# Kernel optimization log

Hardware: AMD Instinct MI355X
Metric: run time of the kernel (lower is better)

Reference implementation:

```python
import jax, jax.numpy as jnp
import numpy as np

N = 20000      # nodes
E = 160000     # edges (before self loops)
IN = 128       # in_channels (== edge_dim)
H = 8          # heads
C = 64         # out_channels per head
NEG_SLOPE = 0.2


def setup_inputs() -> dict:
    key = jax.random.key(0)
    ks = jax.random.split(key, 8)
    s_in = np.float32(1.0 / np.sqrt(IN))
    s_att = np.float32(1.0 / np.sqrt(C))
    return {
        "x": jax.random.normal(ks[0], (N, IN), jnp.float32),
        "edge_index": jax.random.randint(ks[1], (2, E), 0, N, dtype=jnp.int32),
        "edge_attr": jax.random.normal(ks[2], (E, IN), jnp.float32),
        "Wl": jax.random.normal(ks[3], (IN, H * C), jnp.float32) * s_in,
        "Wr": jax.random.normal(ks[4], (IN, H * C), jnp.float32) * s_in,
        "We": jax.random.normal(ks[5], (IN, H * C), jnp.float32) * s_in,
        "att": jax.random.normal(ks[6], (H, C), jnp.float32) * s_att,
        "bias": jnp.zeros((H * C,), jnp.float32),
    }


def reference(x, edge_index, edge_attr, Wl, Wr, We, att, bias):
    n = x.shape[0]
    e = edge_attr.shape[0]
    src, dst = edge_index[0], edge_index[1]

    # add self loops; self-loop edge_attr = per-target-node mean of incoming
    # edge attrs (PyG fill_value='mean'); nodes with no in-edges get zeros.
    cnt = jax.ops.segment_sum(jnp.ones((e,), x.dtype), dst, num_segments=n)
    loop_attr = jax.ops.segment_sum(edge_attr, dst, num_segments=n) / jnp.maximum(cnt, 1.0)[:, None]
    loops = jnp.arange(n, dtype=src.dtype)
    src_f = jnp.concatenate([src, loops])          # [E+N]
    dst_f = jnp.concatenate([dst, loops])          # [E+N]
    ea = jnp.concatenate([edge_attr, loop_attr], axis=0)  # [E+N, IN]

    xl = (x @ Wl).reshape(n, H, C)   # source projection
    xr = (x @ Wr).reshape(n, H, C)   # target projection
    xe = (ea @ We).reshape(-1, H, C)  # edge projection

    # GATv2 score: att . LeakyReLU(xl_j + xr_i + xe)
    m = jax.nn.leaky_relu(xl[src_f] + xr[dst_f] + xe, NEG_SLOPE)  # [E+N, H, C]
    logits = jnp.einsum('ehc,hc->eh', m, att)                      # [E+N, H]

    # segment softmax over incoming edges of each target node
    lmax = jax.ops.segment_max(logits, dst_f, num_segments=n)      # [N, H]
    p = jnp.exp(logits - lmax[dst_f])
    denom = jax.ops.segment_sum(p, dst_f, num_segments=n)
    alpha = p / denom[dst_f]                                       # [E+N, H]

    # weighted scatter-add aggregation of source features
    out = jax.ops.segment_sum(alpha[:, :, None] * xl[src_f], dst_f, num_segments=n)
    return out.reshape(n, H * C) + bias
```

## Files before the change

### kernel.cpp

```cpp
#include <hip/hip_runtime.h>

#define N_NODES 20000
#define E_EDGES 160000
#define IN_CH 128
#define H_HEADS 8
#define C_CH 64
#define HC 512
#define M_TOT (E_EDGES + N_NODES)
#define NEG_SLOPE 0.2f
#define NCHUNK ((N_NODES + 255) / 256)

typedef __attribute__((ext_vector_type(8))) short bf16x8;
typedef __attribute__((ext_vector_type(4))) float f32x4;

__device__ __forceinline__ unsigned short f2bf(float f) {
    unsigned u = __float_as_uint(f);
    unsigned r = (u + 0x7FFFu + ((u >> 16) & 1u)) >> 16;
    return (unsigned short)r;
}
__device__ __forceinline__ float bf2f(unsigned short s) {
    return __uint_as_float((unsigned)s << 16);
}
__device__ __forceinline__ float bfx(const bf16x8& v0, const bf16x8& v1, int idx) {
    return bf2f((unsigned short)((idx < 8) ? v0[idx] : v1[idx - 8]));
}

#define GLOAD_LDS16(gsrc, ldst) \
    __builtin_amdgcn_global_load_lds((const __attribute__((address_space(1))) void*)(gsrc), \
                                     (__attribute__((address_space(3))) void*)(ldst), 16, 0, 0)

__global__ void k_deg(const int* __restrict__ ei, int* __restrict__ deg) {
    int e = blockIdx.x * blockDim.x + threadIdx.x;
    if (e >= E_EDGES) return;
    atomicAdd(&deg[ei[E_EDGES + e]], 1);
}

__global__ void k_scan1(const int* __restrict__ deg, int* __restrict__ bsum) {
    __shared__ int red[256];
    int tid = threadIdx.x;
    int i = blockIdx.x * 256 + tid;
    red[tid] = (i < N_NODES) ? deg[i] + 1 : 0;
    __syncthreads();
    for (int off = 128; off > 0; off >>= 1) {
        if (tid < off) red[tid] += red[tid + off];
        __syncthreads();
    }
    if (tid == 0) bsum[blockIdx.x] = red[0];
}

__global__ void k_scan2(const int* __restrict__ bsum, int* __restrict__ boff) {
    if (threadIdx.x == 0) {
        int run = 0;
        for (int b = 0; b < NCHUNK; ++b) { boff[b] = run; run += bsum[b]; }
    }
}

__global__ void k_scan3(const int* __restrict__ deg, const int* __restrict__ boff,
                        int* __restrict__ rowptr, int* __restrict__ cursor,
                        int* __restrict__ eidx, int* __restrict__ src_s,
                        int* __restrict__ dst_s) {
    __shared__ int buf[256];
    int tid = threadIdx.x;
    int i = blockIdx.x * 256 + tid;
    int v = (i < N_NODES) ? deg[i] + 1 : 0;
    buf[tid] = v;
    __syncthreads();
    for (int off = 1; off < 256; off <<= 1) {
        int tv = (tid >= off) ? buf[tid - off] : 0;
        __syncthreads();
        buf[tid] += tv;
        __syncthreads();
    }
    if (i < N_NODES) {
        int excl = boff[blockIdx.x] + buf[tid] - v;
        rowptr[i] = excl;
        eidx[excl] = E_EDGES + i;
        src_s[excl] = i;
        dst_s[excl] = i;
        cursor[i] = excl + 1;
        if (i == N_NODES - 1) rowptr[N_NODES] = excl + v;
    }
}

__global__ void k_fill(const int* __restrict__ ei, int* __restrict__ cursor,
                       int* __restrict__ eidx, int* __restrict__ src_s,
                       int* __restrict__ dst_s) {
    int e = blockIdx.x * blockDim.x + threadIdx.x;
    if (e >= E_EDGES) return;
    int d = ei[E_EDGES + e];
    int slot = atomicAdd(&cursor[d], 1);
    eidx[slot] = e;
    src_s[slot] = ei[e];
    dst_s[slot] = d;
}

__global__ void k_prep(const int* __restrict__ rowptr, const int* __restrict__ eidx,
                       const float* __restrict__ ea, unsigned short* __restrict__ eab) {
    int node = (blockIdx.x * blockDim.x + threadIdx.x) >> 6;
    int lane = threadIdx.x & 63;
    if (node >= N_NODES) return;
    int beg = rowptr[node], end = rowptr[node + 1];
    int cnt = end - beg - 1;
    float s0 = 0.f, s1 = 0.f;
    if (beg + 1 < end) {
        const float* p_nxt = ea + (size_t)eidx[beg + 1] * 128 + lane;
        for (int p = beg + 1; p < end; ++p) {
            const float* cur = p_nxt;
            if (p + 1 < end) p_nxt = ea + (size_t)eidx[p + 1] * 128 + lane;
            float v0 = cur[0], v1 = cur[64];
            s0 += v0; s1 += v1;
            eab[(size_t)p * 128 + lane] = f2bf(v0);
            eab[(size_t)p * 128 + 64 + lane] = f2bf(v1);
        }
    }
    float inv = 1.f / fmaxf((float)cnt, 1.f);
    eab[(size_t)beg * 128 + lane] = f2bf(s0 * inv);
    eab[(size_t)beg * 128 + 64 + lane] = f2bf(s1 * inv);
}

__global__ void k_trans3(const float* __restrict__ Wl, const float* __restrict__ Wr,
                         const float* __restrict__ We,
                         unsigned short* __restrict__ WlT, unsigned short* __restrict__ WrT,
                         unsigned short* __restrict__ WeT) {
    int idx = blockIdx.x * blockDim.x + threadIdx.x;
    if (idx >= HC * IN_CH) return;
    int m = blockIdx.y;
    const float* W = (m == 0) ? Wl : (m == 1) ? Wr : We;
    unsigned short* WT = (m == 0) ? WlT : (m == 1) ? WrT : WeT;
    int n = idx >> 7, k = idx & 127;
    WT[idx] = f2bf(W[(size_t)k * HC + n]);
}

__global__ void k_gemm2(const float* __restrict__ A,
                        const unsigned short* __restrict__ WlT,
                        const unsigned short* __restrict__ WrT,
                        unsigned short* __restrict__ xlb, unsigned short* __restrict__ xrb,
                        int M) {
    __shared__ short As[64 * 128];
    int row0 = blockIdx.x * 64;
    int sel = blockIdx.y >> 1;
    const unsigned short* BT = sel ? WrT : WlT;
    unsigned short* Cb = sel ? xrb : xlb;
    int t = threadIdx.x;
    {
        int row = t >> 2, c0 = (t & 3) * 32;
        int gr = row0 + row;
        int sw = (row & 7) << 4;
        const float* src = A + (size_t)gr * 128 + c0;
        #pragma unroll
        for (int i = 0; i < 4; ++i) {
            bf16x8 v;
            if (gr < M) {
                const float4* p = (const float4*)(src + i * 8);
                float4 f0 = p[0], f1 = p[1];
                v[0] = f2bf(f0.x); v[1] = f2bf(f0.y); v[2] = f2bf(f0.z); v[3] = f2bf(f0.w);
                v[4] = f2bf(f1.x); v[5] = f2bf(f1.y); v[6] = f2bf(f1.z); v[7] = f2bf(f1.w);
            } else {
                #pragma unroll
                for (int j = 0; j < 8; ++j) v[j] = 0;
            }
            int off = row * 256 + (((c0 + i * 8) * 2) ^ sw);
            *(bf16x8*)((char*)As + off) = v;
        }
    }
    __syncthreads();

    int w = t >> 6, l = t & 63;
    int lr = l & 15, lk = l >> 4;
    int col0 = (blockIdx.y & 1) * 256 + w * 64;

    f32x4 acc[4][4];
    #pragma unroll
    for (int mi = 0; mi < 4; ++mi)
        #pragma unroll
        for (int fj = 0; fj < 4; ++fj)
            #pragma unroll
            for (int q = 0; q < 4; ++q) acc[mi][fj][q] = 0.f;

    #pragma unroll
    for (int k0 = 0; k0 < 4; ++k0) {
        bf16x8 a4[4];
        #pragma unroll
        for (int mi = 0; mi < 4; ++mi) {
            int row = mi * 16 + lr;
            int off = row * 256 + ((k0 * 64 + lk * 16) ^ ((row & 7) << 4));
            a4[mi] = *(const bf16x8*)((const char*)As + off);
        }
        #pragma unroll
        for (int fj = 0; fj < 4; ++fj) {
            bf16x8 b = *(const bf16x8*)(BT + (size_t)(col0 + fj * 16 + lr) * 128 + k0 * 32 + lk * 8);
            #pragma unroll
            for (int mi = 0; mi < 4; ++mi)
                acc[mi][fj] = __builtin_amdgcn_mfma_f32_16x16x32_bf16(a4[mi], b, acc[mi][fj], 0, 0, 0);
        }
    }
    #pragma unroll
    for (int mi = 0; mi < 4; ++mi) {
        #pragma unroll
        for (int reg = 0; reg < 4; ++reg) {
            int r = row0 + mi * 16 + lk * 4 + reg;
            if (r < M) {
                unsigned short* cp = Cb + (size_t)r * 512 + col0 + lr;
                #pragma unroll
                for (int fj = 0; fj < 4; ++fj) cp[fj * 16] = f2bf(acc[mi][fj][reg]);
            }
        }
    }
}

#define PREF(R, CB, SLOT) { \
    int s_ = s_src[R], d_ = s_dst[R]; \
    const bf16x8* xp_ = (const bf16x8*)(xlb + (size_t)s_ * 512 + (CB) + q * 16); \
    pa0[SLOT] = xp_[0]; pa1[SLOT] = xp_[1]; \
    const bf16x8* rp_ = (const bf16x8*)(xrb + (size_t)d_ * 512 + (CB) + q * 16); \
    pb0[SLOT] = rp_[0]; pb1[SLOT] = rp_[1]; }

__global__ void k_fused(const int* __restrict__ src_s, const int* __restrict__ dst_s,
                        const int* __restrict__ rowptr,
                        const unsigned short* __restrict__ eab,
                        const unsigned short* __restrict__ WeT,
                        const unsigned short* __restrict__ xlb,
                        const unsigned short* __restrict__ xrb,
                        const float* __restrict__ att, const float* __restrict__ bias,
                        float* __restrict__ logits, float* __restrict__ out) {
    __shared__ short As[64 * 128];
    __shared__ float xeT[4][16][68];
    __shared__ float att_s[512];
    __shared__ float lg[64][8];
    __shared__ int s_src[64], s_dst[64];
    __shared__ int own_node[64], own_beg[64], own_len[64];
    __shared__ int n_own;
    int row0 = blockIdx.x * 64;
    int t = threadIdx.x;

    if (t == 0) n_own = 0;
    __syncthreads();

    {
        int l = t & 63;
        int c_base = (t >> 6) * 4;
        #pragma unroll
        for (int i = 0; i < 4; ++i) {
            int c = c_base + i;
            int row_local = c * 4 + (l >> 4);
            int grow = row0 + row_local;
            if (grow > M_TOT - 1) grow = M_TOT - 1;
            int chunk = (l & 15) ^ (row_local & 7);
            const char* src = (const char*)eab + (size_t)grow * 256 + chunk * 16;
            char* dst = (char*)As + c * 1024;
            GLOAD_LDS16(src, dst);
        }
    }

    if (t < 64) {
        int p = row0 + t;
        int s = 0, d = 0;
        if (p < M_TOT) {
            s = src_s[p]; d = dst_s[p];
            int pb = rowptr[d], pe = rowptr[d + 1];
            if (pb == p && pe <= row0 + 64) {
                int idx = atomicAdd(&n_own, 1);
                own_node[idx] = d; own_beg[idx] = t; own_len[idx] = pe - pb;
            }
        }
        s_src[t] = s; s_dst[t] = d;
    }
    att_s[t] = att[t];
    att_s[t + 256] = att[t + 256];

    asm volatile("s_waitcnt vmcnt(0)");
    __syncthreads();

    int w = t >> 6, l = t & 63;
    int lr = l & 15, lk = l >> 4;
    int eloc = l >> 2, q = l & 3;
    int cb0 = w * 128;

    bf16x8 pa0[2], pa1[2], pb0[2], pb1[2];
    f32x4 acc[4][4];

    PREF(eloc, cb0, 0);

    #pragma unroll
    for (int hh = 0; hh < 2; ++hh) {
        int cb = cb0 + hh * 64;
        int h = w * 2 + hh;

        #pragma unroll
        for (int mi = 0; mi < 4; ++mi)
            #pragma unroll
            for (int fj = 0; fj < 4; ++fj)
                #pragma unroll
                for (int qq = 0; qq < 4; ++qq) acc[mi][fj][qq] = 0.f;

        #pragma unroll
        for (int k0 = 0; k0 < 4; ++k0) {
            bf16x8 a4[4];
            #pragma unroll
            for (int mi = 0; mi < 4; ++mi) {
                int row = mi * 16 + lr;
                int off = row * 256 + ((k0 * 64 + lk * 16) ^ ((row & 7) << 4));
                a4[mi] = *(const bf16x8*)((const char*)As + off);
            }
            #pragma unroll
            for (int fj = 0; fj < 4; ++fj) {
                bf16x8 b = *(const bf16x8*)(WeT + (size_t)(cb + fj * 16 + lr) * 128 + k0 * 32 + lk * 8);
                #pragma unroll
                for (int mi = 0; mi < 4; ++mi)
                    acc[mi][fj] = __builtin_amdgcn_mfma_f32_16x16x32_bf16(a4[mi], b, acc[mi][fj], 0, 0, 0);
            }
        }

        #pragma unroll
        for (int mi = 0; mi < 4; ++mi) {
            if (mi < 3) { PREF(mi * 16 + 16 + eloc, cb, (mi + 1) & 1); }
            else if (hh == 0) { PREF(eloc, cb + 64, 0); }

            #pragma unroll
            for (int fj = 0; fj < 4; ++fj)
                #pragma unroll
                for (int reg = 0; reg < 4; ++reg)
                    xeT[w][lk * 4 + reg][fj * 16 + lr] = acc[mi][fj][reg];

            const bf16x8 ca0 = pa0[mi & 1], ca1 = pa1[mi & 1];
            const bf16x8 cb0v = pb0[mi & 1], cb1v = pb1[mi & 1];

            float sum = 0.f;
            #pragma unroll
            for (int sg = 0; sg < 4; ++sg) {
                float4 xe4 = *(const float4*)&xeT[w][eloc][q * 16 + sg * 4];
                float4 av  = *(const float4*)&att_s[cb + q * 16 + sg * 4];
                float v0 = xe4.x + bfx(ca0, ca1, sg * 4 + 0) + bfx(cb0v, cb1v, sg * 4 + 0);
                float v1 = xe4.y + bfx(ca0, ca1, sg * 4 + 1) + bfx(cb0v, cb1v, sg * 4 + 1);
                float v2 = xe4.z + bfx(ca0, ca1, sg * 4 + 2) + bfx(cb0v, cb1v, sg * 4 + 2);
                float v3 = xe4.w + bfx(ca0, ca1, sg * 4 + 3) + bfx(cb0v, cb1v, sg * 4 + 3);
                v0 = (v0 > 0.f) ? v0 : v0 * NEG_SLOPE;
                v1 = (v1 > 0.f) ? v1 : v1 * NEG_SLOPE;
                v2 = (v2 > 0.f) ? v2 : v2 * NEG_SLOPE;
                v3 = (v3 > 0.f) ? v3 : v3 * NEG_SLOPE;
                sum = fmaf(av.x, v0, sum);
                sum = fmaf(av.y, v1, sum);
                sum = fmaf(av.z, v2, sum);
                sum = fmaf(av.w, v3, sum);
            }
            sum += __shfl_xor(sum, 1, 64);
            sum += __shfl_xor(sum, 2, 64);
            if (q == 0) {
                int rloc = mi * 16 + eloc;
                lg[rloc][h] = sum;
                int p = row0 + rloc;
                if (p < M_TOT) logits[(size_t)p * 8 + h] = sum;
            }
        }
    }
    __syncthreads();

    {
        int lane = t & 63;
        int h = lane >> 3;
        for (int o = w; o < n_own; o += 4) {
            int d = own_node[o], rb = own_beg[o], len = own_len[o];
            float m = -3.4e38f;
            for (int j = 0; j < len; ++j) m = fmaxf(m, lg[rb + j][h]);
            float den = 0.f;
            for (int j = 0; j < len; ++j) den += __expf(lg[rb + j][h] - m);
            float rden = 1.f / den;
            float ac[8] = {};
            bf16x8 v_nxt = *(const bf16x8*)(xlb + (size_t)s_src[rb] * 512 + lane * 8);
            for (int j = 0; j < len; ++j) {
                bf16x8 v = v_nxt;
                if (j + 1 < len)
                    v_nxt = *(const bf16x8*)(xlb + (size_t)s_src[rb + j + 1] * 512 + lane * 8);
                float alpha = __expf(lg[rb + j][h] - m) * rden;
                #pragma unroll
                for (int jj = 0; jj < 8; ++jj) ac[jj] = fmaf(alpha, bf2f((unsigned short)v[jj]), ac[jj]);
            }
            float4* op = (float4*)(out + (size_t)d * 512 + lane * 8);
            const float4* bp = (const float4*)(bias + lane * 8);
            float4 bv0 = bp[0], bv1 = bp[1];
            float4 r0 = { ac[0] + bv0.x, ac[1] + bv0.y, ac[2] + bv0.z, ac[3] + bv0.w };
            float4 r1 = { ac[4] + bv1.x, ac[5] + bv1.y, ac[6] + bv1.z, ac[7] + bv1.w };
            op[0] = r0; op[1] = r1;
        }
    }
}

__global__ void k_cleanup(const int* __restrict__ rowptr, const int* __restrict__ src_s,
                          const float* __restrict__ logits,
                          const unsigned short* __restrict__ xlb, const float* __restrict__ bias,
                          float* __restrict__ out) {
    int node = (blockIdx.x * blockDim.x + threadIdx.x) >> 6;
    int lane = threadIdx.x & 63;
    if (node >= N_NODES) return;
    int beg = rowptr[node], end = rowptr[node + 1];
    if ((beg >> 6) == ((end - 1) >> 6)) return;
    int h = lane >> 3;

    float m = -3.4e38f;
    for (int p = beg; p < end; ++p) m = fmaxf(m, logits[(size_t)p * 8 + h]);
    float den = 0.f;
    for (int p = beg; p < end; ++p) den += __expf(logits[(size_t)p * 8 + h] - m);
    float rden = 1.f / den;

    float acc[8] = {};
    bf16x8 v_nxt = *(const bf16x8*)(xlb + (size_t)src_s[beg] * 512 + lane * 8);
    for (int p = beg; p < end; ++p) {
        bf16x8 v = v_nxt;
        float lgv = logits[(size_t)p * 8 + h];
        if (p + 1 < end)
            v_nxt = *(const bf16x8*)(xlb + (size_t)src_s[p + 1] * 512 + lane * 8);
        float alpha = __expf(lgv - m) * rden;
        #pragma unroll
        for (int j = 0; j < 8; ++j) acc[j] = fmaf(alpha, bf2f((unsigned short)v[j]), acc[j]);
    }
    float4* op = (float4*)(out + (size_t)node * 512 + lane * 8);
    const float4* bp = (const float4*)(bias + lane * 8);
    float4 bv0 = bp[0], bv1 = bp[1];
    float4 r0 = { acc[0] + bv0.x, acc[1] + bv0.y, acc[2] + bv0.z, acc[3] + bv0.w };
    float4 r1 = { acc[4] + bv1.x, acc[5] + bv1.y, acc[6] + bv1.z, acc[7] + bv1.w };
    op[0] = r0; op[1] = r1;
}

extern "C" void kernel_launch(void* const* d_in, const int* in_sizes, int n_in,
                              void* d_out, int out_size, void* d_ws, size_t ws_size,
                              hipStream_t stream) {
    const float* x    = (const float*)d_in[0];
    const int*   ei   = (const int*)d_in[1];
    const float* ea   = (const float*)d_in[2];
    const float* Wl   = (const float*)d_in[3];
    const float* Wr   = (const float*)d_in[4];
    const float* We   = (const float*)d_in[5];
    const float* att  = (const float*)d_in[6];
    const float* bias = (const float*)d_in[7];
    float* out = (float*)d_out;

    unsigned short* xlb = (unsigned short*)d_ws;
    unsigned short* xrb = xlb + (size_t)N_NODES * HC;
    unsigned short* WlT = xrb + (size_t)N_NODES * HC;
    unsigned short* WrT = WlT + HC * IN_CH;
    unsigned short* WeT = WrT + HC * IN_CH;
    unsigned short* eab = WeT + HC * IN_CH;
    float* logits    = (float*)(eab + (size_t)M_TOT * IN_CH);
    int* deg         = (int*)(logits + (size_t)M_TOT * 8);
    int* rowptr      = deg + N_NODES;
    int* cursor      = rowptr + N_NODES + 1;
    int* eidx        = cursor + N_NODES;
    int* src_s       = eidx + M_TOT;
    int* dst_s       = src_s + M_TOT;
    int* bsum        = dst_s + M_TOT;
    int* boff        = bsum + NCHUNK;

    const int B = 256;
    hipMemsetAsync(deg, 0, N_NODES * sizeof(int), stream);
    k_deg<<<(E_EDGES + B - 1) / B, B, 0, stream>>>(ei, deg);
    k_scan1<<<NCHUNK, B, 0, stream>>>(deg, bsum);
    k_scan2<<<1, 64, 0, stream>>>(bsum, boff);
    k_scan3<<<NCHUNK, B, 0, stream>>>(deg, boff, rowptr, cursor, eidx, src_s, dst_s);
    k_fill<<<(E_EDGES + B - 1) / B, B, 0, stream>>>(ei, cursor, eidx, src_s, dst_s);
    k_prep<<<(N_NODES * 64 + B - 1) / B, B, 0, stream>>>(rowptr, eidx, ea, eab);
    k_trans3<<<dim3((HC * IN_CH + B - 1) / B, 3), B, 0, stream>>>(Wl, Wr, We, WlT, WrT, WeT);
    k_gemm2<<<dim3((N_NODES + 63) / 64, 4), B, 0, stream>>>(x, WlT, WrT, xlb, xrb, N_NODES);
    k_fused<<<(M_TOT + 63) / 64, B, 0, stream>>>(src_s, dst_s, rowptr, eab, WeT,
                                                 xlb, xrb, att, bias, logits, out);
    k_cleanup<<<((size_t)N_NODES * 64 + B - 1) / B, B, 0, stream>>>(rowptr, src_s, logits,
                                                                    xlb, bias, out);
}
```

Baseline: 262.8 us.

## Split edge-attr prep across two waves, merge gemm column halves, store xe as bf16

k_prep now assigns two wavefronts per node, one per 64-channel half, and prefetches two edges ahead to raise parallelism and memory-level concurrency. k_gemm2 computes both 256-column halves in one block, so the A tile is converted and staged into LDS once instead of twice. In k_fused the edge projection tile is staged in LDS as truncated bf16 rather than fp32, which halves the LDS footprint and read traffic. The truncation adds rounding error to the attention logits.

```diff
diff --git a/kernel.cpp b/kernel.cpp
--- a/kernel.cpp
+++ b/kernel.cpp
@@ -17,6 +17,9 @@
     unsigned u = __float_as_uint(f);
     unsigned r = (u + 0x7FFFu + ((u >> 16) & 1u)) >> 16;
     return (unsigned short)r;
+}
+__device__ __forceinline__ unsigned short f2bf_trunc(float f) {
+    return (unsigned short)(__float_as_uint(f) >> 16);
 }
 __device__ __forceinline__ float bf2f(unsigned short s) {
     return __uint_as_float((unsigned)s << 16);
@@ -96,26 +99,25 @@
 
 __global__ void k_prep(const int* __restrict__ rowptr, const int* __restrict__ eidx,
                        const float* __restrict__ ea, unsigned short* __restrict__ eab) {
-    int node = (blockIdx.x * blockDim.x + threadIdx.x) >> 6;
+    int gid = (blockIdx.x * blockDim.x + threadIdx.x) >> 6;
+    int node = gid >> 1;
+    int half = gid & 1;
     int lane = threadIdx.x & 63;
     if (node >= N_NODES) return;
-    int beg = rowptr[node], end = rowptr[node + 1];
-    int cnt = end - beg - 1;
-    float s0 = 0.f, s1 = 0.f;
-    if (beg + 1 < end) {
-        const float* p_nxt = ea + (size_t)eidx[beg + 1] * 128 + lane;
-        for (int p = beg + 1; p < end; ++p) {
-            const float* cur = p_nxt;
-            if (p + 1 < end) p_nxt = ea + (size_t)eidx[p + 1] * 128 + lane;
-            float v0 = cur[0], v1 = cur[64];
-            s0 += v0; s1 += v1;
-            eab[(size_t)p * 128 + lane] = f2bf(v0);
-            eab[(size_t)p * 128 + 64 + lane] = f2bf(v1);
-        }
-    }
-    float inv = 1.f / fmaxf((float)cnt, 1.f);
-    eab[(size_t)beg * 128 + lane] = f2bf(s0 * inv);
-    eab[(size_t)beg * 128 + 64 + lane] = f2bf(s1 * inv);
+    int c = half * 64 + lane;
+    int beg = rowptr[node] + 1, end = rowptr[node + 1];
+    float s = 0.f;
+    float v0 = 0.f, v1 = 0.f;
+    if (beg < end)     v0 = ea[(size_t)eidx[beg] * 128 + c];
+    if (beg + 1 < end) v1 = ea[(size_t)eidx[beg + 1] * 128 + c];
+    for (int p = beg; p < end; ++p) {
+        float cur = v0;
+        v0 = v1;
+        if (p + 2 < end) v1 = ea[(size_t)eidx[p + 2] * 128 + c];
+        s += cur;
+        eab[(size_t)p * 128 + c] = f2bf(cur);
+    }
+    eab[(size_t)(beg - 1) * 128 + c] = f2bf(s / fmaxf((float)(end - beg), 1.f));
 }
 
 __global__ void k_trans3(const float* __restrict__ Wl, const float* __restrict__ Wr,
@@ -138,7 +140,7 @@
                         int M) {
     __shared__ short As[64 * 128];
     int row0 = blockIdx.x * 64;
-    int sel = blockIdx.y >> 1;
+    int sel = blockIdx.y;
     const unsigned short* BT = sel ? WrT : WlT;
     unsigned short* Cb = sel ? xrb : xlb;
     int t = threadIdx.x;
@@ -167,42 +169,45 @@
 
     int w = t >> 6, l = t & 63;
     int lr = l & 15, lk = l >> 4;
-    int col0 = (blockIdx.y & 1) * 256 + w * 64;
-
-    f32x4 acc[4][4];
+
     #pragma unroll
-    for (int mi = 0; mi < 4; ++mi)
-        #pragma unroll
-        for (int fj = 0; fj < 4; ++fj)
-            #pragma unroll
-            for (int q = 0; q < 4; ++q) acc[mi][fj][q] = 0.f;
-
-    #pragma unroll
-    for (int k0 = 0; k0 < 4; ++k0) {
-        bf16x8 a4[4];
+    for (int ch = 0; ch < 2; ++ch) {
+        int col0 = ch * 256 + w * 64;
+        f32x4 acc[4][4];
+        #pragma unroll
+        for (int mi = 0; mi < 4; ++mi)
+            #pragma unroll
+            for (int fj = 0; fj < 4; ++fj)
+                #pragma unroll
+                for (int q = 0; q < 4; ++q) acc[mi][fj][q] = 0.f;
+
+        #pragma unroll
+        for (int k0 = 0; k0 < 4; ++k0) {
+            bf16x8 a4[4];
+            #pragma unroll
+            for (int mi = 0; mi < 4; ++mi) {
+                int row = mi * 16 + lr;
+                int off = row * 256 + ((k0 * 64 + lk * 16) ^ ((row & 7) << 4));
+                a4[mi] = *(const bf16x8*)((const char*)As + off);
+            }
+            #pragma unroll
+            for (int fj = 0; fj < 4; ++fj) {
+                bf16x8 b = *(const bf16x8*)(BT + (size_t)(col0 + fj * 16 + lr) * 128 + k0 * 32 + lk * 8);
+                #pragma unroll
+                for (int mi = 0; mi < 4; ++mi)
+                    acc[mi][fj] = __builtin_amdgcn_mfma_f32_16x16x32_bf16(a4[mi], b, acc[mi][fj], 0, 0, 0);
+            }
+        }
         #pragma unroll
         for (int mi = 0; mi < 4; ++mi) {
-            int row = mi * 16 + lr;
-            int off = row * 256 + ((k0 * 64 + lk * 16) ^ ((row & 7) << 4));
-            a4[mi] = *(const bf16x8*)((const char*)As + off);
-        }
-        #pragma unroll
-        for (int fj = 0; fj < 4; ++fj) {
-            bf16x8 b = *(const bf16x8*)(BT + (size_t)(col0 + fj * 16 + lr) * 128 + k0 * 32 + lk * 8);
-            #pragma unroll
-            for (int mi = 0; mi < 4; ++mi)
-                acc[mi][fj] = __builtin_amdgcn_mfma_f32_16x16x32_bf16(a4[mi], b, acc[mi][fj], 0, 0, 0);
-        }
-    }
-    #pragma unroll
-    for (int mi = 0; mi < 4; ++mi) {
-        #pragma unroll
-        for (int reg = 0; reg < 4; ++reg) {
-            int r = row0 + mi * 16 + lk * 4 + reg;
-            if (r < M) {
-                unsigned short* cp = Cb + (size_t)r * 512 + col0 + lr;
-                #pragma unroll
-                for (int fj = 0; fj < 4; ++fj) cp[fj * 16] = f2bf(acc[mi][fj][reg]);
+            #pragma unroll
+            for (int reg = 0; reg < 4; ++reg) {
+                int r = row0 + mi * 16 + lk * 4 + reg;
+                if (r < M) {
+                    unsigned short* cp = Cb + (size_t)r * 512 + col0 + lr;
+                    #pragma unroll
+                    for (int fj = 0; fj < 4; ++fj) cp[fj * 16] = f2bf(acc[mi][fj][reg]);
+                }
             }
         }
     }
@@ -224,7 +229,7 @@
                         const float* __restrict__ att, const float* __restrict__ bias,
                         float* __restrict__ logits, float* __restrict__ out) {
     __shared__ short As[64 * 128];
-    __shared__ float xeT[4][16][68];
+    __shared__ unsigned short xeT[4][16][72];
     __shared__ float att_s[512];
     __shared__ float lg[64][8];
     __shared__ int s_src[64], s_dst[64];
@@ -320,20 +325,22 @@
             for (int fj = 0; fj < 4; ++fj)
                 #pragma unroll
                 for (int reg = 0; reg < 4; ++reg)
-                    xeT[w][lk * 4 + reg][fj * 16 + lr] = acc[mi][fj][reg];
+                    xeT[w][lk * 4 + reg][fj * 16 + lr] = f2bf_trunc(acc[mi][fj][reg]);
 
             const bf16x8 ca0 = pa0[mi & 1], ca1 = pa1[mi & 1];
             const bf16x8 cb0v = pb0[mi & 1], cb1v = pb1[mi & 1];
 
+            bf16x8 x0 = *(const bf16x8*)&xeT[w][eloc][q * 16];
+            bf16x8 x1 = *(const bf16x8*)&xeT[w][eloc][q * 16 + 8];
+
             float sum = 0.f;
             #pragma unroll
             for (int sg = 0; sg < 4; ++sg) {
-                float4 xe4 = *(const float4*)&xeT[w][eloc][q * 16 + sg * 4];
-                float4 av  = *(const float4*)&att_s[cb + q * 16 + sg * 4];
-                float v0 = xe4.x + bfx(ca0, ca1, sg * 4 + 0) + bfx(cb0v, cb1v, sg * 4 + 0);
-                float v1 = xe4.y + bfx(ca0, ca1, sg * 4 + 1) + bfx(cb0v, cb1v, sg * 4 + 1);
-                float v2 = xe4.z + bfx(ca0, ca1, sg * 4 + 2) + bfx(cb0v, cb1v, sg * 4 + 2);
-                float v3 = xe4.w + bfx(ca0, ca1, sg * 4 + 3) + bfx(cb0v, cb1v, sg * 4 + 3);
+                float4 av = *(const float4*)&att_s[cb + q * 16 + sg * 4];
+                float v0 = bfx(x0, x1, sg * 4 + 0) + bfx(ca0, ca1, sg * 4 + 0) + bfx(cb0v, cb1v, sg * 4 + 0);
+                float v1 = bfx(x0, x1, sg * 4 + 1) + bfx(ca0, ca1, sg * 4 + 1) + bfx(cb0v, cb1v, sg * 4 + 1);
+                float v2 = bfx(x0, x1, sg * 4 + 2) + bfx(ca0, ca1, sg * 4 + 2) + bfx(cb0v, cb1v, sg * 4 + 2);
+                float v3 = bfx(x0, x1, sg * 4 + 3) + bfx(ca0, ca1, sg * 4 + 3) + bfx(cb0v, cb1v, sg * 4 + 3);
                 v0 = (v0 > 0.f) ? v0 : v0 * NEG_SLOPE;
                 v1 = (v1 > 0.f) ? v1 : v1 * NEG_SLOPE;
                 v2 = (v2 > 0.f) ? v2 : v2 * NEG_SLOPE;
@@ -457,9 +464,9 @@
     k_scan2<<<1, 64, 0, stream>>>(bsum, boff);
     k_scan3<<<NCHUNK, B, 0, stream>>>(deg, boff, rowptr, cursor, eidx, src_s, dst_s);
     k_fill<<<(E_EDGES + B - 1) / B, B, 0, stream>>>(ei, cursor, eidx, src_s, dst_s);
-    k_prep<<<(N_NODES * 64 + B - 1) / B, B, 0, stream>>>(rowptr, eidx, ea, eab);
+    k_prep<<<((size_t)N_NODES * 128 + B - 1) / B, B, 0, stream>>>(rowptr, eidx, ea, eab);
     k_trans3<<<dim3((HC * IN_CH + B - 1) / B, 3), B, 0, stream>>>(Wl, Wr, We, WlT, WrT, WeT);
-    k_gemm2<<<dim3((N_NODES + 63) / 64, 4), B, 0, stream>>>(x, WlT, WrT, xlb, xrb, N_NODES);
+    k_gemm2<<<dim3((N_NODES + 63) / 64, 2), B, 0, stream>>>(x, WlT, WrT, xlb, xrb, N_NODES);
     k_fused<<<(M_TOT + 63) / 64, B, 0, stream>>>(src_s, dst_s, rowptr, eab, WeT,
                                                  xlb, xrb, att, bias, logits, out);
     k_cleanup<<<((size_t)N_NODES * 64 + B - 1) / B, B, 0, stream>>>(rowptr, src_s, logits,
```

Measured after the change: 289.4 us. 1.1x slower.
